# Performance work log

Hardware: AMD Instinct MI355X
Metric: run time of the kernel (lower is better)

## Reference

```python
import jax, jax.numpy as jnp
import numpy as np


def setup_inputs() -> dict:
    key = jax.random.key(0)
    k1, k2 = jax.random.split(key)
    B, C, H, W = 8, 32, 384, 384
    # probability-map-like predictions in [0, 1)
    pred = jax.random.uniform(k1, (B, C, H, W), dtype=jnp.float32)
    target = jax.random.randint(k2, (B, H, W), 0, C)  # int labels, all classes present w.h.p.
    return {"pred": pred, "target": target}


def reference(pred, target):
    """J-statistic loss (arXiv:1910.09783). reduction='none', weights=ones.

    Original computes, for each ci != ck:
      loss[b,ci,ck] = w[ci,ck] * log(0.5 + sum_hw pred[b,ci]*(phi[b,ci]-phi[b,ck])/2)
    where phi = one_hot(target)/n_i. The O(C^2) loop collapses to a single
    batched contraction S[b,i,k] = <pred[b,i], phi[b,k]> over spatial dims.
    """
    B, C, H, W = pred.shape
    t1h = jax.nn.one_hot(target, C, dtype=pred.dtype)          # (B,H,W,C)
    t1h = jnp.moveaxis(t1h, -1, 1)                             # (B,C,H,W)
    n_i = t1h.sum(axis=(-2, -1))[:, :, None, None]             # (B,C,1,1) class pixel counts
    phi = t1h / n_i                                            # normalized one-hot
    # S[b,i,k] = sum_hw pred[b,i]*phi[b,k]
    S = jnp.einsum('bihw,bkhw->bik', pred, phi)                # (B,C,C)
    diag = jnp.diagonal(S, axis1=1, axis2=2)                   # (B,C) = S[b,i,i]
    delta_sum = (diag[:, :, None] - S) * 0.5                   # sum_hw pred_i * (phi_i - phi_k)/2
    weights = jnp.ones((C, C), dtype=pred.dtype)
    loss = weights * jnp.log(0.5 + delta_sum)                  # (B,C,C)
    off_diag = 1.0 - jnp.eye(C, dtype=pred.dtype)              # skip ci == ck terms
    j = -(loss * off_diag).sum(axis=(-2, -1))                  # (B,)
    return j
```

## Files before the change

### kernel.cpp

```cpp
#include <hip/hip_runtime.h>


#define BB 8
#define CC 32
#define HW 147456
#define PX_BLK 256
#define NCHUNK (HW / PX_BLK)
#define STRIDE 258

typedef __attribute__((ext_vector_type(8))) short short8;
typedef __attribute__((ext_vector_type(4))) float float4v;
typedef __attribute__((ext_vector_type(4))) unsigned uint4v;

__device__ __forceinline__ unsigned pk(float lo, float hi) {
    return __builtin_amdgcn_perm(__float_as_uint(hi), __float_as_uint(lo), 0x07060302u);
}
__device__ __forceinline__ unsigned oh2(int ta, int tb, int m) {
    return (ta == m ? 0x3F80u : 0u) | (tb == m ? 0x3F800000u : 0u);
}

__global__ __launch_bounds__(256, 4) void jloss_mfma(
    const float* __restrict__ pred,
    const int*   __restrict__ target,
    float*       __restrict__ T,
    float*       __restrict__ cnt)
{
    __shared__ float tile[CC * STRIDE];

    const int tid  = threadIdx.x;
    const int w    = tid >> 6;
    const int l    = tid & 63;
    const int quad = l >> 4;
    const int m    = l & 15;
    const int blk  = blockIdx.x;
    const int b    = blk / NCHUNK;
    const int chunk= blk % NCHUNK;

    const long px0 = (long)chunk * PX_BLK;
    const float* predb = pred + (long)b * CC * HW;
    const int*   tgtb  = target + (long)b * HW;

    #pragma unroll
    for (int r = 0; r < 8; ++r) {
        const int c = w * 8 + r;
        const float* gp = predb + (long)c * HW + px0 + l * 4;
        __builtin_amdgcn_global_load_lds(
            (const __attribute__((address_space(1))) void*)gp,
            (__attribute__((address_space(3))) void*)&tile[c * STRIDE + l * 4],
            16, 0, 0);
    }
    __syncthreads();

    float4v acc00 = {0,0,0,0}, acc01 = {0,0,0,0};
    float4v acc10 = {0,0,0,0}, acc11 = {0,0,0,0};
    float4v accc0 = {0,0,0,0}, accc1 = {0,0,0,0};
    const short8 ONES = {0x3F80,0x3F80,0x3F80,0x3F80,0x3F80,0x3F80,0x3F80,0x3F80};

    #pragma unroll
    for (int kk = 0; kk < 2; ++kk) {
        const int ks   = w * 2 + kk;
        const int base = ks * 32 + quad * 8;
        const float2* r0 = (const float2*)&tile[m * STRIDE + base];
        const float2* r1 = (const float2*)&tile[(m + 16) * STRIDE + base];
        const float2 x0 = r0[0], x1 = r0[1], x2 = r0[2], x3 = r0[3];
        const float2 y0 = r1[0], y1 = r1[1], y2 = r1[2], y3 = r1[3];
        const int4 t0 = *(const int4*)(tgtb + px0 + base);
        const int4 t1 = *(const int4*)(tgtb + px0 + base + 4);

        union { short8 s; uint4v u; } A0, A1, B0, B1;
        A0.u[0] = pk(x0.x, x0.y); A0.u[1] = pk(x1.x, x1.y);
        A0.u[2] = pk(x2.x, x2.y); A0.u[3] = pk(x3.x, x3.y);
        A1.u[0] = pk(y0.x, y0.y); A1.u[1] = pk(y1.x, y1.y);
        A1.u[2] = pk(y2.x, y2.y); A1.u[3] = pk(y3.x, y3.y);
        B0.u[0] = oh2(t0.x, t0.y, m);      B0.u[1] = oh2(t0.z, t0.w, m);
        B0.u[2] = oh2(t1.x, t1.y, m);      B0.u[3] = oh2(t1.z, t1.w, m);
        const int m16 = m + 16;
        B1.u[0] = oh2(t0.x, t0.y, m16);    B1.u[1] = oh2(t0.z, t0.w, m16);
        B1.u[2] = oh2(t1.x, t1.y, m16);    B1.u[3] = oh2(t1.z, t1.w, m16);

        acc00 = __builtin_amdgcn_mfma_f32_16x16x32_bf16(A0.s, B0.s, acc00, 0, 0, 0);
        acc01 = __builtin_amdgcn_mfma_f32_16x16x32_bf16(A0.s, B1.s, acc01, 0, 0, 0);
        acc10 = __builtin_amdgcn_mfma_f32_16x16x32_bf16(A1.s, B0.s, acc10, 0, 0, 0);
        acc11 = __builtin_amdgcn_mfma_f32_16x16x32_bf16(A1.s, B1.s, acc11, 0, 0, 0);
        accc0 = __builtin_amdgcn_mfma_f32_16x16x32_bf16(ONES, B0.s, accc0, 0, 0, 0);
        accc1 = __builtin_amdgcn_mfma_f32_16x16x32_bf16(ONES, B1.s, accc1, 0, 0, 0);
    }
    __syncthreads();

    float (*red)[CC][CC] = (float (*)[CC][CC])tile;
    float* redc = tile + 4 * CC * CC;
    #pragma unroll
    for (int r = 0; r < 4; ++r) {
        red[w][quad*4 + r     ][m     ] = acc00[r];
        red[w][quad*4 + r     ][m + 16] = acc01[r];
        red[w][quad*4 + r + 16][m     ] = acc10[r];
        red[w][quad*4 + r + 16][m + 16] = acc11[r];
    }
    if (quad == 0) {
        redc[w * CC + m]      = accc0[0];
        redc[w * CC + m + 16] = accc1[0];
    }
    __syncthreads();

    float* Tb = T + (long)b * CC * CC;
    const float* rp = &red[0][0][0];
    for (int j = tid; j < CC * CC; j += 256) {
        const float s = rp[j] + rp[1024 + j] + rp[2048 + j] + rp[3072 + j];
        atomicAdd(&Tb[j], s);
    }
    if (tid < CC)
        atomicAdd(&cnt[b * CC + tid],
                  redc[tid] + redc[CC + tid] + redc[2*CC + tid] + redc[3*CC + tid]);
}

__global__ __launch_bounds__(256) void jloss_final(
    const float* __restrict__ T,
    const float* __restrict__ cnt,
    float*       __restrict__ out)
{
    const int b   = blockIdx.x;
    const int tid = threadIdx.x;
    __shared__ float diag_s[CC];
    __shared__ float inv_n[CC];
    __shared__ float wsum[4];

    const float* Tb = T + (long)b * CC * CC;
    const float* cb = cnt + b * CC;

    if (tid < CC) {
        const float inv = 1.0f / cb[tid];
        inv_n[tid]  = inv;
        diag_s[tid] = Tb[tid * CC + tid] * inv;
    }
    __syncthreads();

    float sum = 0.0f;
    for (int idx = tid; idx < CC * CC; idx += 256) {
        const int i = idx >> 5;
        const int k = idx & 31;
        if (i != k) {
            const float S = Tb[idx] * inv_n[k];
            sum += logf(0.5f + 0.5f * (diag_s[i] - S));
        }
    }
    #pragma unroll
    for (int off = 32; off > 0; off >>= 1) sum += __shfl_down(sum, off, 64);
    if ((tid & 63) == 0) wsum[tid >> 6] = sum;
    __syncthreads();
    if (tid == 0) out[b] = -(wsum[0] + wsum[1] + wsum[2] + wsum[3]);
}

extern "C" void kernel_launch(void* const* d_in, const int* in_sizes, int n_in,
                              void* d_out, int out_size, void* d_ws, size_t ws_size,
                              hipStream_t stream) {
    const float* pred   = (const float*)d_in[0];
    const int*   target = (const int*)d_in[1];
    float* out = (float*)d_out;

    float* T   = (float*)d_ws;
    float* cnt = (float*)d_ws + BB * CC * CC;

    hipMemsetAsync(d_ws, 0, (BB * CC * CC + BB * CC) * sizeof(float), stream);

    jloss_mfma <<<BB * NCHUNK, 256, 0, stream>>>(pred, target, T, cnt);
    jloss_final<<<BB, 256, 0, stream>>>(T, cnt, out);
}
```

Baseline: 236.8 us.

## Process four sub-tiles per block and replace atomics with a partial-sum reduction

Each block now loops over four 256-pixel sub-tiles, so there are four times fewer blocks and the accumulators are reused across more pixels. Instead of atomically adding 1056 floats per block into a shared result, each block writes its own partial slice and a new reduce kernel sums the partials per batch. This removes the memset, the atomic contention and the per-block reduction overhead. In exchange it adds an extra kernel launch and serializes load and compute within each block, since there is no double buffering across sub-tiles.

```diff
diff --git a/kernel.cpp b/kernel.cpp
--- a/kernel.cpp
+++ b/kernel.cpp
@@ -4,9 +4,11 @@
 #define BB 8
 #define CC 32
 #define HW 147456
-#define PX_BLK 256
-#define NCHUNK (HW / PX_BLK)
+#define CHUNK_PX 1024
+#define SUB_PX 256
+#define NCHUNK (HW / CHUNK_PX)
 #define STRIDE 258
+#define PART (CC * CC + CC)
 
 typedef __attribute__((ext_vector_type(8))) short short8;
 typedef __attribute__((ext_vector_type(4))) float float4v;
@@ -22,8 +24,7 @@
 __global__ __launch_bounds__(256, 4) void jloss_mfma(
     const float* __restrict__ pred,
     const int*   __restrict__ target,
-    float*       __restrict__ T,
-    float*       __restrict__ cnt)
+    float*       __restrict__ P)
 {
     __shared__ float tile[CC * STRIDE];
 
@@ -36,56 +37,65 @@
     const int b    = blk / NCHUNK;
     const int chunk= blk % NCHUNK;
 
-    const long px0 = (long)chunk * PX_BLK;
+    const long px0 = (long)chunk * CHUNK_PX;
     const float* predb = pred + (long)b * CC * HW;
     const int*   tgtb  = target + (long)b * HW;
-
-    #pragma unroll
-    for (int r = 0; r < 8; ++r) {
-        const int c = w * 8 + r;
-        const float* gp = predb + (long)c * HW + px0 + l * 4;
-        __builtin_amdgcn_global_load_lds(
-            (const __attribute__((address_space(1))) void*)gp,
-            (__attribute__((address_space(3))) void*)&tile[c * STRIDE + l * 4],
-            16, 0, 0);
-    }
-    __syncthreads();
 
     float4v acc00 = {0,0,0,0}, acc01 = {0,0,0,0};
     float4v acc10 = {0,0,0,0}, acc11 = {0,0,0,0};
     float4v accc0 = {0,0,0,0}, accc1 = {0,0,0,0};
     const short8 ONES = {0x3F80,0x3F80,0x3F80,0x3F80,0x3F80,0x3F80,0x3F80,0x3F80};
 
-    #pragma unroll
-    for (int kk = 0; kk < 2; ++kk) {
-        const int ks   = w * 2 + kk;
-        const int base = ks * 32 + quad * 8;
-        const float2* r0 = (const float2*)&tile[m * STRIDE + base];
-        const float2* r1 = (const float2*)&tile[(m + 16) * STRIDE + base];
-        const float2 x0 = r0[0], x1 = r0[1], x2 = r0[2], x3 = r0[3];
-        const float2 y0 = r1[0], y1 = r1[1], y2 = r1[2], y3 = r1[3];
-        const int4 t0 = *(const int4*)(tgtb + px0 + base);
-        const int4 t1 = *(const int4*)(tgtb + px0 + base + 4);
+    for (int st = 0; st < 4; ++st) {
+        const long pxs = px0 + st * SUB_PX;
 
-        union { short8 s; uint4v u; } A0, A1, B0, B1;
-        A0.u[0] = pk(x0.x, x0.y); A0.u[1] = pk(x1.x, x1.y);
-        A0.u[2] = pk(x2.x, x2.y); A0.u[3] = pk(x3.x, x3.y);
-        A1.u[0] = pk(y0.x, y0.y); A1.u[1] = pk(y1.x, y1.y);
-        A1.u[2] = pk(y2.x, y2.y); A1.u[3] = pk(y3.x, y3.y);
-        B0.u[0] = oh2(t0.x, t0.y, m);      B0.u[1] = oh2(t0.z, t0.w, m);
-        B0.u[2] = oh2(t1.x, t1.y, m);      B0.u[3] = oh2(t1.z, t1.w, m);
-        const int m16 = m + 16;
-        B1.u[0] = oh2(t0.x, t0.y, m16);    B1.u[1] = oh2(t0.z, t0.w, m16);
-        B1.u[2] = oh2(t1.x, t1.y, m16);    B1.u[3] = oh2(t1.z, t1.w, m16);
+        #pragma unroll
+        for (int r = 0; r < 8; ++r) {
+            const int c = w * 8 + r;
+            const float* gp = predb + (long)c * HW + pxs + l * 4;
+            __builtin_amdgcn_global_load_lds(
+                (const __attribute__((address_space(1))) void*)gp,
+                (__attribute__((address_space(3))) void*)&tile[c * STRIDE + l * 4],
+                16, 0, 0);
+        }
+        const int base0 = (w * 2    ) * 32 + quad * 8;
+        const int base1 = (w * 2 + 1) * 32 + quad * 8;
+        const int4 t0a = *(const int4*)(tgtb + pxs + base0);
+        const int4 t0b = *(const int4*)(tgtb + pxs + base0 + 4);
+        const int4 t1a = *(const int4*)(tgtb + pxs + base1);
+        const int4 t1b = *(const int4*)(tgtb + pxs + base1 + 4);
+        __syncthreads();
 
-        acc00 = __builtin_amdgcn_mfma_f32_16x16x32_bf16(A0.s, B0.s, acc00, 0, 0, 0);
-        acc01 = __builtin_amdgcn_mfma_f32_16x16x32_bf16(A0.s, B1.s, acc01, 0, 0, 0);
-        acc10 = __builtin_amdgcn_mfma_f32_16x16x32_bf16(A1.s, B0.s, acc10, 0, 0, 0);
-        acc11 = __builtin_amdgcn_mfma_f32_16x16x32_bf16(A1.s, B1.s, acc11, 0, 0, 0);
-        accc0 = __builtin_amdgcn_mfma_f32_16x16x32_bf16(ONES, B0.s, accc0, 0, 0, 0);
-        accc1 = __builtin_amdgcn_mfma_f32_16x16x32_bf16(ONES, B1.s, accc1, 0, 0, 0);
+        #pragma unroll
+        for (int kk = 0; kk < 2; ++kk) {
+            const int base = kk ? base1 : base0;
+            const int4 ta = kk ? t1a : t0a;
+            const int4 tb = kk ? t1b : t0b;
+            const float2* r0 = (const float2*)&tile[m * STRIDE + base];
+            const float2* r1 = (const float2*)&tile[(m + 16) * STRIDE + base];
+            const float2 x0 = r0[0], x1 = r0[1], x2 = r0[2], x3 = r0[3];
+            const float2 y0 = r1[0], y1 = r1[1], y2 = r1[2], y3 = r1[3];
+
+            union { short8 s; uint4v u; } A0, A1, B0, B1;
+            A0.u[0] = pk(x0.x, x0.y); A0.u[1] = pk(x1.x, x1.y);
+            A0.u[2] = pk(x2.x, x2.y); A0.u[3] = pk(x3.x, x3.y);
+            A1.u[0] = pk(y0.x, y0.y); A1.u[1] = pk(y1.x, y1.y);
+            A1.u[2] = pk(y2.x, y2.y); A1.u[3] = pk(y3.x, y3.y);
+            B0.u[0] = oh2(ta.x, ta.y, m);   B0.u[1] = oh2(ta.z, ta.w, m);
+            B0.u[2] = oh2(tb.x, tb.y, m);   B0.u[3] = oh2(tb.z, tb.w, m);
+            const int m16 = m + 16;
+            B1.u[0] = oh2(ta.x, ta.y, m16); B1.u[1] = oh2(ta.z, ta.w, m16);
+            B1.u[2] = oh2(tb.x, tb.y, m16); B1.u[3] = oh2(tb.z, tb.w, m16);
+
+            acc00 = __builtin_amdgcn_mfma_f32_16x16x32_bf16(A0.s, B0.s, acc00, 0, 0, 0);
+            acc01 = __builtin_amdgcn_mfma_f32_16x16x32_bf16(A0.s, B1.s, acc01, 0, 0, 0);
+            acc10 = __builtin_amdgcn_mfma_f32_16x16x32_bf16(A1.s, B0.s, acc10, 0, 0, 0);
+            acc11 = __builtin_amdgcn_mfma_f32_16x16x32_bf16(A1.s, B1.s, acc11, 0, 0, 0);
+            accc0 = __builtin_amdgcn_mfma_f32_16x16x32_bf16(ONES, B0.s, accc0, 0, 0, 0);
+            accc1 = __builtin_amdgcn_mfma_f32_16x16x32_bf16(ONES, B1.s, accc1, 0, 0, 0);
+        }
+        __syncthreads();
     }
-    __syncthreads();
 
     float (*red)[CC][CC] = (float (*)[CC][CC])tile;
     float* redc = tile + 4 * CC * CC;
@@ -102,20 +112,31 @@
     }
     __syncthreads();
 
-    float* Tb = T + (long)b * CC * CC;
+    float* Pb = P + (long)blk * PART;
     const float* rp = &red[0][0][0];
-    for (int j = tid; j < CC * CC; j += 256) {
-        const float s = rp[j] + rp[1024 + j] + rp[2048 + j] + rp[3072 + j];
-        atomicAdd(&Tb[j], s);
-    }
+    #pragma unroll
+    for (int j = tid; j < CC * CC; j += 256)
+        Pb[j] = rp[j] + rp[1024 + j] + rp[2048 + j] + rp[3072 + j];
     if (tid < CC)
-        atomicAdd(&cnt[b * CC + tid],
-                  redc[tid] + redc[CC + tid] + redc[2*CC + tid] + redc[3*CC + tid]);
+        Pb[CC * CC + tid] = redc[tid] + redc[CC + tid] + redc[2*CC + tid] + redc[3*CC + tid];
+}
+
+__global__ __launch_bounds__(256) void jloss_reduce(
+    const float* __restrict__ P,
+    float*       __restrict__ Tn)
+{
+    const int gid = blockIdx.x * 256 + threadIdx.x;
+    const int b   = gid / PART;
+    const int j   = gid % PART;
+    const float* Pb = P + (long)b * NCHUNK * PART + j;
+    float s = 0.0f;
+    #pragma unroll 8
+    for (int c = 0; c < NCHUNK; ++c) s += Pb[(long)c * PART];
+    Tn[gid] = s;
 }
 
 __global__ __launch_bounds__(256) void jloss_final(
-    const float* __restrict__ T,
-    const float* __restrict__ cnt,
+    const float* __restrict__ Tn,
     float*       __restrict__ out)
 {
     const int b   = blockIdx.x;
@@ -124,8 +145,8 @@
     __shared__ float inv_n[CC];
     __shared__ float wsum[4];
 
-    const float* Tb = T + (long)b * CC * CC;
-    const float* cb = cnt + b * CC;
+    const float* Tb = Tn + (long)b * PART;
+    const float* cb = Tb + CC * CC;
 
     if (tid < CC) {
         const float inv = 1.0f / cb[tid];
@@ -156,12 +177,10 @@
     const float* pred   = (const float*)d_in[0];
     const int*   target = (const int*)d_in[1];
     float* out = (float*)d_out;
+    float* P   = (float*)d_ws;
+    float* Tn  = (float*)d_ws + (long)BB * NCHUNK * PART;
 
-    float* T   = (float*)d_ws;
-    float* cnt = (float*)d_ws + BB * CC * CC;
-
-    hipMemsetAsync(d_ws, 0, (BB * CC * CC + BB * CC) * sizeof(float), stream);
-
-    jloss_mfma <<<BB * NCHUNK, 256, 0, stream>>>(pred, target, T, cnt);
-    jloss_final<<<BB, 256, 0, stream>>>(T, cnt, out);
+    jloss_mfma  <<<BB * NCHUNK, 256, 0, stream>>>(pred, target, P);
+    jloss_reduce<<<(BB * PART) / 256, 256, 0, stream>>>(P, Tn);
+    jloss_final <<<BB, 256, 0, stream>>>(Tn, out);
 }
```

Measured after the change: 229.6 us. 3.1% less time.
